# Performance work log

Measured on AMD Instinct MI355X. Metric: run time of the kernel, lower is better.

The kernel has to match this reference:

```python
import jax, jax.numpy as jnp
import numpy as np

B, NPTS, NBOX = 16, 100000, 64
PTS_THRESHOLD = 2048          # topk voxels kept per scene
GT_THRESHOLD = 2.5            # distance multiplier
VOXEL_SIZE = 0.01
TENSOR_STRIDE = 8             # stride of the level being pruned
SIZE = TENSOR_STRIDE * VOXEL_SIZE  # 0.08, per-voxel cell size at this level


def setup_inputs() -> dict:
    key = jax.random.key(0)
    k1, k2, k3 = jax.random.split(key, 3)
    scores = jax.random.normal(k1, (B, NPTS), dtype=jnp.float32)
    points = jax.random.uniform(k2, (B, NPTS, 3), dtype=jnp.float32)
    gt_centers = jax.random.uniform(k3, (B, NBOX, 3), dtype=jnp.float32)
    return {"scores": scores, "points": points, "gt_centers": gt_centers}


def reference(scores, points, gt_centers):
    # --- per-batch topk score mask (MEFPN3D._get_score_mask) ---
    _, idx = jax.lax.top_k(scores, PTS_THRESHOLD)          # [B, K]
    score_mask = jnp.zeros(scores.shape, dtype=bool)
    score_mask = score_mask.at[jnp.arange(B)[:, None], idx].set(True)  # scatter True

    # --- gt distance mask (MEFPN3D._get_gt_mask) ---
    # distances: [B, Npts, n_boxes]
    diff = points[:, :, None, :] - gt_centers[:, None, :, :]
    distances = jnp.sqrt(jnp.sum(diff * diff, axis=-1))
    gt_mask = jnp.any(distances < SIZE * GT_THRESHOLD, axis=-1)        # [B, Npts]

    # --- combined prune mask (scatter of per-batch masks into global mask) ---
    prune_mask = jnp.logical_or(score_mask, gt_mask)

    # --- per-voxel sigmoid BCE loss, reduction='none' (CrossEntropyLoss use_sigmoid=True) ---
    target = gt_mask.astype(scores.dtype)
    losses = target * jax.nn.softplus(-scores) + (1.0 - target) * jax.nn.softplus(scores)
    return prune_mask, losses
```

## Files before the change

kernel.cpp:

```cpp
#include <hip/hip_runtime.h>
#include <hip/hip_bf16.h>
#include <stdint.h>

#define BB 16
#define NPTS 100000
#define NBOX 64
#define KTOP 2048
#define THRF 0.2f
#define C_LO 0.039984f
#define C_HI 0.040016f

#define HSLICES 98
#define SLICE_PTS 1024

#define VALS_OFF  0
#define HISTG_OFF (BB * HSLICES * 1024)
#define PREFG_OFF (HISTG_OFF + BB * HSLICES * 256)
#define STATE_OFF (PREFG_OFF + BB * HSLICES * 256)
#define LIST_CAP 8192

__device__ __forceinline__ uint32_t fmap(float f) {
    uint32_t b = __float_as_uint(f);
    return (b & 0x80000000u) ? ~b : (b | 0x80000000u);
}

__global__ __launch_bounds__(256) void bucket_k(const float* __restrict__ scores,
                                                uint32_t* __restrict__ ws) {
    __shared__ uint32_t wh[4][256];
    __shared__ uint32_t htmp[256];
    __shared__ uint32_t excl[256];
    __shared__ uint32_t wcur[4][256];
    __shared__ uint32_t sorted[SLICE_PTS];
    const int b = blockIdx.y, sl = blockIdx.x;
    const int tid = threadIdx.x, w = tid >> 6, lane = tid & 63;
#pragma unroll
    for (int j = 0; j < 4; ++j) wh[j][tid] = 0;
    __syncthreads();
    const int p0 = sl * SLICE_PTS + tid * 4;
    uint32_t u[4];
    const bool valid = p0 < NPTS;
    if (valid) {
        const float4 v = *reinterpret_cast<const float4*>(scores + (size_t)b * NPTS + p0);
        u[0] = fmap(v.x); u[1] = fmap(v.y); u[2] = fmap(v.z); u[3] = fmap(v.w);
#pragma unroll
        for (int j = 0; j < 4; ++j) atomicAdd(&wh[w][u[j] >> 24], 1u);
    }
    __syncthreads();
    const uint32_t c0 = wh[0][tid], c1 = wh[1][tid], c2 = wh[2][tid], c3 = wh[3][tid];
    const uint32_t ht = c0 + c1 + c2 + c3;
    htmp[tid] = ht;
    __syncthreads();
    if (tid < 64) {
        const uint32_t v0 = htmp[4*tid], v1 = htmp[4*tid+1], v2 = htmp[4*tid+2], v3 = htmp[4*tid+3];
        const uint32_t lt = v0 + v1 + v2 + v3;
        uint32_t x = lt;
#pragma unroll
        for (int off = 1; off < 64; off <<= 1) {
            const uint32_t y = __shfl_up(x, off);
            if (lane >= off) x += y;
        }
        const uint32_t ex = x - lt;
        excl[4*tid] = ex; excl[4*tid+1] = ex + v0;
        excl[4*tid+2] = ex + v0 + v1; excl[4*tid+3] = ex + v0 + v1 + v2;
    }
    __syncthreads();
    const uint32_t e = excl[tid];
    wcur[0][tid] = e;
    wcur[1][tid] = e + c0;
    wcur[2][tid] = e + c0 + c1;
    wcur[3][tid] = e + c0 + c1 + c2;
    const size_t sb = ((size_t)(b * HSLICES + sl)) * 256;
    ws[HISTG_OFF + sb + tid] = ht;
    ws[PREFG_OFF + sb + tid] = e;
    __syncthreads();
    if (valid) {
#pragma unroll
        for (int j = 0; j < 4; ++j) {
            const uint32_t pos = atomicAdd(&wcur[w][u[j] >> 24], 1u);
            sorted[pos] = u[j];
        }
    }
    __syncthreads();
    const int n = min(SLICE_PTS, NPTS - sl * SLICE_PTS);
    uint32_t* gv = ws + VALS_OFF + ((size_t)(b * HSLICES + sl)) * SLICE_PTS;
    for (int i = tid; i < n; i += 256) gv[i] = sorted[i];
}

__device__ __forceinline__ void wave_select(const uint32_t* __restrict__ h,
                                            uint32_t* __restrict__ pf,
                                            int tid, int lane, uint32_t target,
                                            uint32_t* sBin, uint32_t* sKrem,
                                            uint32_t* sE, uint32_t* sTot) {
    __syncthreads();
    if (tid < 64) {
        const uint32_t v0 = h[4*tid], v1 = h[4*tid+1], v2 = h[4*tid+2], v3 = h[4*tid+3];
        const uint32_t lt = v0 + v1 + v2 + v3;
        uint32_t x = lt;
#pragma unroll
        for (int off = 1; off < 64; off <<= 1) {
            const uint32_t y = __shfl_up(x, off);
            if (lane >= off) x += y;
        }
        const uint32_t ex = x - lt;
        pf[4*tid] = ex; pf[4*tid+1] = ex + v0;
        pf[4*tid+2] = ex + v0 + v1; pf[4*tid+3] = ex + v0 + v1 + v2;
        if (tid == 63) *sTot = x;
    }
    __syncthreads();
    if (tid < 256) {
        const uint32_t total = *sTot, lim = total - target;
        const uint32_t pe = pf[tid];
        const uint32_t pe1 = (tid == 255) ? total : pf[tid + 1];
        if (pe <= lim && pe1 > lim) {
            *sBin = (uint32_t)tid;
            *sKrem = target - (total - pe1);
            *sE = pe1 - pe;
        }
    }
    __syncthreads();
}

__global__ __launch_bounds__(1024) void select_k(const float* __restrict__ scores,
                                                 uint32_t* __restrict__ ws) {
    const int b = blockIdx.x, tid = threadIdx.x, lane = tid & 63, wid = tid >> 6;
    __shared__ uint32_t hsum[4][256];
    __shared__ uint32_t hist[256];
    __shared__ uint32_t pf[256];
    __shared__ uint32_t lens[HSLICES], starts[HSLICES], outoff[HSLICES];
    __shared__ uint32_t list[LIST_CAP];
    __shared__ uint32_t sBin, sKrem, sE, sTot, sCnt, sIstar, sRun;

    {
        const int g = tid >> 8, t = tid & 255;
        const int s0 = g * 25, s1 = (g == 3) ? HSLICES : (s0 + 25);
        uint32_t acc = 0;
        for (int s = s0; s < s1; ++s)
            acc += ws[HISTG_OFF + ((size_t)(b * HSLICES + s)) * 256 + t];
        hsum[g][t] = acc;
    }
    if (tid == 0) sIstar = NPTS;
    __syncthreads();
    if (tid < 256) hist[tid] = hsum[0][tid] + hsum[1][tid] + hsum[2][tid] + hsum[3][tid];
    wave_select(hist, pf, tid, lane, KTOP, &sBin, &sKrem, &sE, &sTot);
    uint32_t prefix = sBin << 24;
    const uint32_t beta = sBin;

    if (tid < HSLICES) {
        const size_t sb = ((size_t)(b * HSLICES + tid)) * 256;
        lens[tid] = ws[HISTG_OFF + sb + beta];
        starts[tid] = ws[PREFG_OFF + sb + beta];
    }
    __syncthreads();
    if (tid < 64) {
        uint32_t a = 0, b2 = 0;
        if (tid < 49) { a = lens[2*tid]; if (2*tid + 1 < HSLICES) b2 = lens[2*tid+1]; }
        const uint32_t lt = a + b2;
        uint32_t x = lt;
#pragma unroll
        for (int off = 1; off < 64; off <<= 1) {
            const uint32_t y = __shfl_up(x, off);
            if (lane >= off) x += y;
        }
        const uint32_t ex = x - lt;
        if (tid < 49) { outoff[2*tid] = ex; if (2*tid + 1 < HSLICES) outoff[2*tid+1] = ex + a; }
        if (tid == 63) sCnt = x;
    }
    __syncthreads();
    uint32_t cnt = sCnt;
    if (cnt > LIST_CAP) cnt = LIST_CAP;
    for (int s = wid; s < HSLICES; s += 16) {
        const uint32_t len = lens[s], st = starts[s], oo = outoff[s];
        const uint32_t* gv = ws + VALS_OFF + ((size_t)(b * HSLICES + s)) * SLICE_PTS + st;
        for (uint32_t j = lane; j < len; j += 64) {
            const uint32_t o = oo + j;
            if (o < LIST_CAP) list[o] = gv[j];
        }
    }

#pragma unroll 1
    for (int shift = 16; shift >= 0; shift -= 8) {
        __syncthreads();
        if (tid < 256) hist[tid] = 0;
        __syncthreads();
        const uint32_t hi = prefix >> (shift + 8);
        for (uint32_t i = tid; i < cnt; i += 1024) {
            const uint32_t u = list[i];
            if ((u >> (shift + 8)) == hi)
                atomicAdd(&hist[(u >> shift) & 255u], 1u);
        }
        const uint32_t target = sKrem;
        wave_select(hist, pf, tid, lane, target, &sBin, &sKrem, &sE, &sTot);
        prefix |= sBin << shift;
    }

    const uint32_t R = sKrem, E = sE;
    const uint32_t tbits = (prefix & 0x80000000u) ? (prefix & 0x7fffffffu) : ~prefix;

    if (E != R) {
        __shared__ uint32_t wcnt[16];
        const float T = __uint_as_float(tbits);
        if (tid == 0) sRun = 0;
        __syncthreads();
        const float* s = scores + (size_t)b * NPTS;
        for (int base = 0; base < NPTS; base += 1024) {
            const uint32_t r0 = sRun;
            if (r0 > R) break;
            const int i = base + tid;
            const bool eq = (i < NPTS) && (s[i] == T);
            const unsigned long long mask = __ballot(eq);
            if (lane == 0) wcnt[wid] = (uint32_t)__popcll(mask);
            __syncthreads();
            uint32_t before = 0, total = 0;
            for (int w = 0; w < 16; ++w) {
                const uint32_t c = wcnt[w];
                if (w < wid) before += c;
                total += c;
            }
            if (eq) {
                const uint32_t rank = r0 + before +
                    (uint32_t)__popcll(mask & ((1ull << lane) - 1ull));
                if (rank == R) sIstar = (uint32_t)i;
            }
            __syncthreads();
            if (tid == 0) sRun = r0 + total;
            __syncthreads();
        }
        __syncthreads();
    }
    if (tid == 0) {
        uint32_t* st = ws + STATE_OFF + b * 2;
        st[0] = tbits;
        st[1] = sIstar;
    }
}

__device__ __noinline__ bool exact_gt(float px, float py, float pz,
                                      const float* __restrict__ C) {
    bool hit = false;
#pragma unroll 1
    for (int k = 0; k < NBOX; ++k) {
        float dx = px - C[3 * k + 0];
        float dy = py - C[3 * k + 1];
        float dz = pz - C[3 * k + 2];
        float d2 = __fadd_rn(__fadd_rn(__fmul_rn(dx, dx), __fmul_rn(dy, dy)),
                             __fmul_rn(dz, dz));
        if (__fsqrt_rn(d2) < THRF) hit = true;
    }
    return hit;
}

__global__ __launch_bounds__(256) void main_k(const float* __restrict__ scores,
                                              const float* __restrict__ points,
                                              const float* __restrict__ ctrs,
                                              const uint32_t* __restrict__ ws,
                                              float* __restrict__ out) {
    const int b = blockIdx.y;
    const uint32_t* st = ws + STATE_OFF + b * 2;
    const float T = __uint_as_float(st[0]);
    const uint32_t Istar = st[1];

    const int p0 = blockIdx.x * 1024 + threadIdx.x * 4;
    if (p0 >= NPTS) return;

    const float* P = points + ((size_t)b * NPTS + p0) * 3;
    const float4 a = *reinterpret_cast<const float4*>(P);
    const float4 c4 = *reinterpret_cast<const float4*>(P + 4);
    const float4 e = *reinterpret_cast<const float4*>(P + 8);
    const float px[4] = {a.x, a.w, c4.z, e.y};
    const float py[4] = {a.y, c4.x, c4.w, e.z};
    const float pz[4] = {a.z, c4.y, e.x, e.w};
    float m2[4] = {1e30f, 1e30f, 1e30f, 1e30f};

    const float* C = ctrs + b * NBOX * 3;
#pragma unroll 16
    for (int k = 0; k < NBOX; ++k) {
        const float cx = C[3 * k + 0];
        const float cy = C[3 * k + 1];
        const float cz = C[3 * k + 2];
        const float cc = fmaf(cx, cx, fmaf(cy, cy, cz * cz));
        const float m2x = -2.0f * cx, m2y = -2.0f * cy, m2z = -2.0f * cz;
#pragma unroll
        for (int j = 0; j < 4; ++j) {
            const float t = fmaf(m2x, px[j], fmaf(m2y, py[j], fmaf(m2z, pz[j], cc)));
            m2[j] = fminf(m2[j], t);
        }
    }

    const float4 sv = *reinterpret_cast<const float4*>(scores + (size_t)b * NPTS + p0);
    const float s[4] = {sv.x, sv.y, sv.z, sv.w};
    float pr[4], ls[4];
#pragma unroll
    for (int j = 0; j < 4; ++j) {
        const float pp = fmaf(px[j], px[j], fmaf(py[j], py[j], pz[j] * pz[j]));
        const float m = pp + m2[j];
        bool gt;
        if (m < C_LO) gt = true;
        else if (m >= C_HI) gt = false;
        else gt = exact_gt(px[j], py[j], pz[j], C);
        const bool sm = (s[j] > T) || (s[j] == T && (uint32_t)(p0 + j) < Istar);
        pr[j] = (gt || sm) ? 1.0f : 0.0f;
        const float x = gt ? -s[j] : s[j];
        ls[j] = fmaxf(x, 0.0f) + log1pf(expf(-fabsf(x)));
    }
    float* o0 = out + (size_t)b * NPTS + p0;
    float* o1 = out + (size_t)BB * NPTS + (size_t)b * NPTS + p0;
    *reinterpret_cast<float4*>(o0) = make_float4(pr[0], pr[1], pr[2], pr[3]);
    *reinterpret_cast<float4*>(o1) = make_float4(ls[0], ls[1], ls[2], ls[3]);
}

extern "C" void kernel_launch(void* const* d_in, const int* in_sizes, int n_in,
                              void* d_out, int out_size, void* d_ws, size_t ws_size,
                              hipStream_t stream) {
    const float* scores = (const float*)d_in[0];
    const float* points = (const float*)d_in[1];
    const float* ctrs   = (const float*)d_in[2];
    float* out = (float*)d_out;
    uint32_t* ws = (uint32_t*)d_ws;

    const dim3 gridP(HSLICES, BB);
    bucket_k<<<gridP, 256, 0, stream>>>(scores, ws);
    select_k<<<BB, 1024, 0, stream>>>(scores, ws);
    main_k<<<gridP, 256, 0, stream>>>(scores, points, ctrs, ws, out);
}
```

Measured before the change: 52.14 us.

## Fuse bucket and select kernels via last-block-done atomic counter

Merges the histogram/bucket kernel and the per-batch top-k select kernel into one launch: each slice block bumps an atomic counter, and the last block for a batch performs the radix select with 256 threads, using a binary-search gather into a smaller shared list. This removes one kernel launch and the gap between the two launches, at the cost of a memset and a select phase that now runs on 256 instead of 1024 threads, serialised inside one block. It also vectorises the sorted-slice store and switches the softplus to fast __logf/__expf intrinsics, which may slightly change loss precision. LIST_CAP is halved to 4096, which truncates candidates if the boundary bucket is larger.

```diff
diff --git a/kernel.cpp b/kernel.cpp
--- a/kernel.cpp
+++ b/kernel.cpp
@@ -12,29 +12,34 @@
 
 #define HSLICES 98
 #define SLICE_PTS 1024
+#define LIST_CAP 4096
 
 #define VALS_OFF  0
 #define HISTG_OFF (BB * HSLICES * 1024)
 #define PREFG_OFF (HISTG_OFF + BB * HSLICES * 256)
 #define STATE_OFF (PREFG_OFF + BB * HSLICES * 256)
-#define LIST_CAP 8192
+#define CTR_OFF   (STATE_OFF + BB * 2)
 
 __device__ __forceinline__ uint32_t fmap(float f) {
     uint32_t b = __float_as_uint(f);
     return (b & 0x80000000u) ? ~b : (b | 0x80000000u);
 }
 
-__global__ __launch_bounds__(256) void bucket_k(const float* __restrict__ scores,
-                                                uint32_t* __restrict__ ws) {
-    __shared__ uint32_t wh[4][256];
-    __shared__ uint32_t htmp[256];
-    __shared__ uint32_t excl[256];
-    __shared__ uint32_t wcur[4][256];
-    __shared__ uint32_t sorted[SLICE_PTS];
+__global__ __launch_bounds__(256) void bucket_select_k(const float* __restrict__ scores,
+                                                       uint32_t* __restrict__ ws) {
+    __shared__ union {
+        struct { uint32_t wh[4][256]; uint32_t wcur[4][256]; uint32_t sorted[SLICE_PTS]; } bk;
+        struct { uint32_t list[LIST_CAP]; } sel;
+    } U;
+    __shared__ uint32_t htmp[256], excl[256];
+    __shared__ uint32_t lens[HSLICES], starts[HSLICES], outoff[HSLICES];
+    __shared__ uint32_t sBin, sKrem, sE, sTot, sCnt, sIstar, sRun, sLast;
+
     const int b = blockIdx.y, sl = blockIdx.x;
     const int tid = threadIdx.x, w = tid >> 6, lane = tid & 63;
-#pragma unroll
-    for (int j = 0; j < 4; ++j) wh[j][tid] = 0;
+
+#pragma unroll
+    for (int j = 0; j < 4; ++j) U.bk.wh[j][tid] = 0;
     __syncthreads();
     const int p0 = sl * SLICE_PTS + tid * 4;
     uint32_t u[4];
@@ -43,10 +48,11 @@
         const float4 v = *reinterpret_cast<const float4*>(scores + (size_t)b * NPTS + p0);
         u[0] = fmap(v.x); u[1] = fmap(v.y); u[2] = fmap(v.z); u[3] = fmap(v.w);
 #pragma unroll
-        for (int j = 0; j < 4; ++j) atomicAdd(&wh[w][u[j] >> 24], 1u);
-    }
-    __syncthreads();
-    const uint32_t c0 = wh[0][tid], c1 = wh[1][tid], c2 = wh[2][tid], c3 = wh[3][tid];
+        for (int j = 0; j < 4; ++j) atomicAdd(&U.bk.wh[w][u[j] >> 24], 1u);
+    }
+    __syncthreads();
+    const uint32_t c0 = U.bk.wh[0][tid], c1 = U.bk.wh[1][tid];
+    const uint32_t c2 = U.bk.wh[2][tid], c3 = U.bk.wh[3][tid];
     const uint32_t ht = c0 + c1 + c2 + c3;
     htmp[tid] = ht;
     __syncthreads();
@@ -65,10 +71,10 @@
     }
     __syncthreads();
     const uint32_t e = excl[tid];
-    wcur[0][tid] = e;
-    wcur[1][tid] = e + c0;
-    wcur[2][tid] = e + c0 + c1;
-    wcur[3][tid] = e + c0 + c1 + c2;
+    U.bk.wcur[0][tid] = e;
+    U.bk.wcur[1][tid] = e + c0;
+    U.bk.wcur[2][tid] = e + c0 + c1;
+    U.bk.wcur[3][tid] = e + c0 + c1 + c2;
     const size_t sb = ((size_t)(b * HSLICES + sl)) * 256;
     ws[HISTG_OFF + sb + tid] = ht;
     ws[PREFG_OFF + sb + tid] = e;
@@ -76,79 +82,70 @@
     if (valid) {
 #pragma unroll
         for (int j = 0; j < 4; ++j) {
-            const uint32_t pos = atomicAdd(&wcur[w][u[j] >> 24], 1u);
-            sorted[pos] = u[j];
+            const uint32_t pos = atomicAdd(&U.bk.wcur[w][u[j] >> 24], 1u);
+            U.bk.sorted[pos] = u[j];
         }
     }
     __syncthreads();
     const int n = min(SLICE_PTS, NPTS - sl * SLICE_PTS);
     uint32_t* gv = ws + VALS_OFF + ((size_t)(b * HSLICES + sl)) * SLICE_PTS;
-    for (int i = tid; i < n; i += 256) gv[i] = sorted[i];
-}
-
-__device__ __forceinline__ void wave_select(const uint32_t* __restrict__ h,
-                                            uint32_t* __restrict__ pf,
-                                            int tid, int lane, uint32_t target,
-                                            uint32_t* sBin, uint32_t* sKrem,
-                                            uint32_t* sE, uint32_t* sTot) {
-    __syncthreads();
-    if (tid < 64) {
-        const uint32_t v0 = h[4*tid], v1 = h[4*tid+1], v2 = h[4*tid+2], v3 = h[4*tid+3];
-        const uint32_t lt = v0 + v1 + v2 + v3;
-        uint32_t x = lt;
-#pragma unroll
-        for (int off = 1; off < 64; off <<= 1) {
-            const uint32_t y = __shfl_up(x, off);
-            if (lane >= off) x += y;
-        }
-        const uint32_t ex = x - lt;
-        pf[4*tid] = ex; pf[4*tid+1] = ex + v0;
-        pf[4*tid+2] = ex + v0 + v1; pf[4*tid+3] = ex + v0 + v1 + v2;
-        if (tid == 63) *sTot = x;
-    }
-    __syncthreads();
-    if (tid < 256) {
-        const uint32_t total = *sTot, lim = total - target;
-        const uint32_t pe = pf[tid];
-        const uint32_t pe1 = (tid == 255) ? total : pf[tid + 1];
-        if (pe <= lim && pe1 > lim) {
-            *sBin = (uint32_t)tid;
-            *sKrem = target - (total - pe1);
-            *sE = pe1 - pe;
-        }
-    }
-    __syncthreads();
-}
-
-__global__ __launch_bounds__(1024) void select_k(const float* __restrict__ scores,
-                                                 uint32_t* __restrict__ ws) {
-    const int b = blockIdx.x, tid = threadIdx.x, lane = tid & 63, wid = tid >> 6;
-    __shared__ uint32_t hsum[4][256];
-    __shared__ uint32_t hist[256];
-    __shared__ uint32_t pf[256];
-    __shared__ uint32_t lens[HSLICES], starts[HSLICES], outoff[HSLICES];
-    __shared__ uint32_t list[LIST_CAP];
-    __shared__ uint32_t sBin, sKrem, sE, sTot, sCnt, sIstar, sRun;
-
+    if (n == SLICE_PTS) {
+        reinterpret_cast<uint4*>(gv)[tid] = reinterpret_cast<const uint4*>(U.bk.sorted)[tid];
+    } else {
+        for (int i = tid; i < n; i += 256) gv[i] = U.bk.sorted[i];
+    }
+
+    __threadfence();
+    if (tid == 0) sLast = (atomicAdd(&ws[CTR_OFF + b], 1u) == HSLICES - 1) ? 1u : 0u;
+    __syncthreads();
+    if (!sLast) return;
+    __threadfence();
+
+    if (tid == 0) sIstar = NPTS;
     {
-        const int g = tid >> 8, t = tid & 255;
-        const int s0 = g * 25, s1 = (g == 3) ? HSLICES : (s0 + 25);
+        const uint32_t* hb = ws + HISTG_OFF + (size_t)b * HSLICES * 256;
         uint32_t acc = 0;
-        for (int s = s0; s < s1; ++s)
-            acc += ws[HISTG_OFF + ((size_t)(b * HSLICES + s)) * 256 + t];
-        hsum[g][t] = acc;
-    }
-    if (tid == 0) sIstar = NPTS;
-    __syncthreads();
-    if (tid < 256) hist[tid] = hsum[0][tid] + hsum[1][tid] + hsum[2][tid] + hsum[3][tid];
-    wave_select(hist, pf, tid, lane, KTOP, &sBin, &sKrem, &sE, &sTot);
-    uint32_t prefix = sBin << 24;
-    const uint32_t beta = sBin;
+#pragma unroll 7
+        for (int s = 0; s < HSLICES; ++s) acc += hb[(size_t)s * 256 + tid];
+        htmp[tid] = acc;
+    }
+
+    uint32_t prefix, beta;
+    {
+        __syncthreads();
+        if (tid < 64) {
+            const uint32_t v0 = htmp[4*tid], v1 = htmp[4*tid+1], v2 = htmp[4*tid+2], v3 = htmp[4*tid+3];
+            const uint32_t lt = v0 + v1 + v2 + v3;
+            uint32_t x = lt;
+#pragma unroll
+            for (int off = 1; off < 64; off <<= 1) {
+                const uint32_t y = __shfl_up(x, off);
+                if (lane >= off) x += y;
+            }
+            const uint32_t ex = x - lt;
+            excl[4*tid] = ex; excl[4*tid+1] = ex + v0;
+            excl[4*tid+2] = ex + v0 + v1; excl[4*tid+3] = ex + v0 + v1 + v2;
+            if (tid == 63) sTot = x;
+        }
+        __syncthreads();
+        {
+            const uint32_t total = sTot, lim = total - KTOP;
+            const uint32_t pe = excl[tid];
+            const uint32_t pe1 = (tid == 255) ? total : excl[tid + 1];
+            if (pe <= lim && pe1 > lim) {
+                sBin = (uint32_t)tid;
+                sKrem = KTOP - (total - pe1);
+            }
+        }
+        __syncthreads();
+        beta = sBin;
+        prefix = beta << 24;
+    }
 
     if (tid < HSLICES) {
-        const size_t sb = ((size_t)(b * HSLICES + tid)) * 256;
-        lens[tid] = ws[HISTG_OFF + sb + beta];
-        starts[tid] = ws[PREFG_OFF + sb + beta];
+        const size_t sb2 = ((size_t)(b * HSLICES + tid)) * 256;
+        lens[tid] = ws[HISTG_OFF + sb2 + beta];
+        starts[tid] = ws[PREFG_OFF + sb2 + beta];
     }
     __syncthreads();
     if (tid < 64) {
@@ -168,28 +165,53 @@
     __syncthreads();
     uint32_t cnt = sCnt;
     if (cnt > LIST_CAP) cnt = LIST_CAP;
-    for (int s = wid; s < HSLICES; s += 16) {
-        const uint32_t len = lens[s], st = starts[s], oo = outoff[s];
-        const uint32_t* gv = ws + VALS_OFF + ((size_t)(b * HSLICES + s)) * SLICE_PTS + st;
-        for (uint32_t j = lane; j < len; j += 64) {
-            const uint32_t o = oo + j;
-            if (o < LIST_CAP) list[o] = gv[j];
-        }
+
+    for (uint32_t i = tid; i < cnt; i += 256) {
+        int lo = 0, hi = HSLICES - 1;
+        while (lo < hi) { const int mid = (lo + hi + 1) >> 1; if (outoff[mid] <= i) lo = mid; else hi = mid - 1; }
+        const uint32_t j = i - outoff[lo];
+        U.sel.list[i] = ws[VALS_OFF + ((size_t)(b * HSLICES + lo)) * SLICE_PTS + starts[lo] + j];
     }
 
 #pragma unroll 1
     for (int shift = 16; shift >= 0; shift -= 8) {
         __syncthreads();
-        if (tid < 256) hist[tid] = 0;
-        __syncthreads();
-        const uint32_t hi = prefix >> (shift + 8);
-        for (uint32_t i = tid; i < cnt; i += 1024) {
-            const uint32_t u = list[i];
-            if ((u >> (shift + 8)) == hi)
-                atomicAdd(&hist[(u >> shift) & 255u], 1u);
-        }
-        const uint32_t target = sKrem;
-        wave_select(hist, pf, tid, lane, target, &sBin, &sKrem, &sE, &sTot);
+        htmp[tid] = 0;
+        __syncthreads();
+        const uint32_t hi8 = prefix >> (shift + 8);
+        for (uint32_t i = tid; i < cnt; i += 256) {
+            const uint32_t uu = U.sel.list[i];
+            if ((uu >> (shift + 8)) == hi8)
+                atomicAdd(&htmp[(uu >> shift) & 255u], 1u);
+        }
+        __syncthreads();
+        if (tid < 64) {
+            const uint32_t v0 = htmp[4*tid], v1 = htmp[4*tid+1], v2 = htmp[4*tid+2], v3 = htmp[4*tid+3];
+            const uint32_t lt = v0 + v1 + v2 + v3;
+            uint32_t x = lt;
+#pragma unroll
+            for (int off = 1; off < 64; off <<= 1) {
+                const uint32_t y = __shfl_up(x, off);
+                if (lane >= off) x += y;
+            }
+            const uint32_t ex = x - lt;
+            excl[4*tid] = ex; excl[4*tid+1] = ex + v0;
+            excl[4*tid+2] = ex + v0 + v1; excl[4*tid+3] = ex + v0 + v1 + v2;
+            if (tid == 63) sTot = x;
+        }
+        __syncthreads();
+        {
+            const uint32_t target = sKrem;
+            const uint32_t total = sTot, lim = total - target;
+            const uint32_t pe = excl[tid];
+            const uint32_t pe1 = (tid == 255) ? total : excl[tid + 1];
+            if (pe <= lim && pe1 > lim) {
+                sBin = (uint32_t)tid;
+                sKrem = target - (total - pe1);
+                if (shift == 0) sE = pe1 - pe;
+            }
+        }
+        __syncthreads();
         prefix |= sBin << shift;
     }
 
@@ -197,23 +219,24 @@
     const uint32_t tbits = (prefix & 0x80000000u) ? (prefix & 0x7fffffffu) : ~prefix;
 
     if (E != R) {
-        __shared__ uint32_t wcnt[16];
+        __shared__ uint32_t wcnt2[4];
         const float T = __uint_as_float(tbits);
         if (tid == 0) sRun = 0;
         __syncthreads();
-        const float* s = scores + (size_t)b * NPTS;
-        for (int base = 0; base < NPTS; base += 1024) {
+        const float* sc = scores + (size_t)b * NPTS;
+        const int wid = tid >> 6;
+        for (int base = 0; base < NPTS; base += 256) {
             const uint32_t r0 = sRun;
             if (r0 > R) break;
             const int i = base + tid;
-            const bool eq = (i < NPTS) && (s[i] == T);
+            const bool eq = (i < NPTS) && (sc[i] == T);
             const unsigned long long mask = __ballot(eq);
-            if (lane == 0) wcnt[wid] = (uint32_t)__popcll(mask);
+            if (lane == 0) wcnt2[wid] = (uint32_t)__popcll(mask);
             __syncthreads();
             uint32_t before = 0, total = 0;
-            for (int w = 0; w < 16; ++w) {
-                const uint32_t c = wcnt[w];
-                if (w < wid) before += c;
+            for (int ww = 0; ww < 4; ++ww) {
+                const uint32_t c = wcnt2[ww];
+                if (ww < wid) before += c;
                 total += c;
             }
             if (eq) {
@@ -300,7 +323,7 @@
         const bool sm = (s[j] > T) || (s[j] == T && (uint32_t)(p0 + j) < Istar);
         pr[j] = (gt || sm) ? 1.0f : 0.0f;
         const float x = gt ? -s[j] : s[j];
-        ls[j] = fmaxf(x, 0.0f) + log1pf(expf(-fabsf(x)));
+        ls[j] = fmaxf(x, 0.0f) + __logf(1.0f + __expf(-fabsf(s[j])));
     }
     float* o0 = out + (size_t)b * NPTS + p0;
     float* o1 = out + (size_t)BB * NPTS + (size_t)b * NPTS + p0;
@@ -317,8 +340,9 @@
     float* out = (float*)d_out;
     uint32_t* ws = (uint32_t*)d_ws;
 
+    hipMemsetAsync((char*)d_ws + (size_t)CTR_OFF * 4, 0, BB * 4, stream);
+
     const dim3 gridP(HSLICES, BB);
-    bucket_k<<<gridP, 256, 0, stream>>>(scores, ws);
-    select_k<<<BB, 1024, 0, stream>>>(scores, ws);
+    bucket_select_k<<<gridP, 256, 0, stream>>>(scores, ws);
     main_k<<<gridP, 256, 0, stream>>>(scores, points, ctrs, ws, out);
 }
```

After: 192.6 us. 269% more time.
